# Kernel tuning notes

Hardware: AMD Instinct MI355X
Metric: run time of the kernel (lower is better)

Reference implementation:

```python
import jax, jax.numpy as jnp
import numpy as np

HIDDEN = 768
NUM_HEADS = 12
HEAD_DIM = HIDDEN // NUM_HEADS
B, S = 4, 2048


def setup_inputs() -> dict:
    key = jax.random.key(0)
    ks = jax.random.split(key, 10)
    scale = 1.0 / np.sqrt(HIDDEN)
    return {
        "hidden_states": jax.random.normal(ks[0], (B, S, HIDDEN), dtype=jnp.float32),
        "attention_mask": jnp.ones((B, S), dtype=jnp.float32),
        "Wq": jax.random.normal(ks[1], (HIDDEN, HIDDEN), dtype=jnp.float32) * scale,
        "bq": jnp.zeros((HIDDEN,), dtype=jnp.float32),
        "Wk": jax.random.normal(ks[2], (HIDDEN, HIDDEN), dtype=jnp.float32) * scale,
        "bk": jnp.zeros((HIDDEN,), dtype=jnp.float32),
        "Wv": jax.random.normal(ks[3], (HIDDEN, HIDDEN), dtype=jnp.float32) * scale,
        "bv": jnp.zeros((HIDDEN,), dtype=jnp.float32),
        "Wo": jax.random.normal(ks[4], (HIDDEN, HIDDEN), dtype=jnp.float32) * scale,
        "bo": jnp.zeros((HIDDEN,), dtype=jnp.float32),
    }


def reference(hidden_states, attention_mask, Wq, bq, Wk, bk, Wv, bv, Wo, bo):
    b, s, _ = hidden_states.shape
    # nn.Linear: x @ W.T + b  (W is [out, in])
    Q = hidden_states @ Wq.T + bq
    K = hidden_states @ Wk.T + bk
    V = hidden_states @ Wv.T + bv
    # [b, s, h*d] -> [b, h, s, d]
    Q = Q.reshape(b, s, NUM_HEADS, HEAD_DIM).transpose(0, 2, 1, 3)
    K = K.reshape(b, s, NUM_HEADS, HEAD_DIM).transpose(0, 2, 1, 3)
    V = V.reshape(b, s, NUM_HEADS, HEAD_DIM).transpose(0, 2, 1, 3)
    # scores: [b, h, s, s]
    scores = jnp.einsum("bhqd,bhkd->bhqk", Q, K) / jnp.sqrt(
        jnp.asarray(HEAD_DIM, dtype=Q.dtype))
    # mask: [b, s] -> additive bias broadcast over heads and query dim
    bias = (1.0 - attention_mask)[:, None, None, :] * -10000.0
    scores = scores + bias
    probs = jax.nn.softmax(scores, axis=-1)  # dropout p=0.0 -> identity
    context = jnp.einsum("bhqk,bhkd->bhqd", probs, V)
    context = context.transpose(0, 2, 1, 3).reshape(b, s, HIDDEN)
    return context @ Wo.T + bo
```

## Files before the change

### kernel.cpp

```cpp
#include <hip/hip_runtime.h>
#include <hip/hip_bf16.h>

#define SEQ   2048
#define NH    12
#define MTOK  8192

typedef __attribute__((ext_vector_type(8))) short short8;
typedef __attribute__((ext_vector_type(4))) short short4v;
typedef __attribute__((ext_vector_type(4))) float f32x4;

__device__ inline short f2bf(float x) {
  __hip_bfloat16 h = __float2bfloat16(x);
  return *(short*)&h;
}

#define GLL(gp, lp) __builtin_amdgcn_global_load_lds( \
    (const __attribute__((address_space(1))) void*)(gp), \
    (__attribute__((address_space(3))) void*)(lp), 16, 0, 0)

#define MFMA(a, b, c) __builtin_amdgcn_mfma_f32_16x16x32_bf16(a, b, c, 0, 0, 0)

#if !defined(__HIP_DEVICE_COMPILE__)
#define MFMA16(a, b, c) (c)
#elif __has_builtin(__builtin_amdgcn_mfma_f32_16x16x16bf16_1k)
#define MFMA16(a, b, c) __builtin_amdgcn_mfma_f32_16x16x16bf16_1k(a, b, c, 0, 0, 0)
#elif __has_builtin(__builtin_amdgcn_mfma_f32_16x16x16_bf16)
#define MFMA16(a, b, c) __builtin_amdgcn_mfma_f32_16x16x16_bf16(a, b, c, 0, 0, 0)
#else
#error "no 16x16x16 bf16 mfma builtin on device"
#endif

#if !defined(__HIP_DEVICE_COMPILE__)
#define EXP2(x) (x)
#elif __has_builtin(__builtin_amdgcn_exp2f)
#define EXP2(x) __builtin_amdgcn_exp2f(x)
#else
#define EXP2(x) __expf((x) * 0.6931471805599453f)
#endif

__device__ inline unsigned pack2bf(float a, float b) {
  unsigned ua = __float_as_uint(a) + 0x8000u;
  unsigned ub = __float_as_uint(b) + 0x8000u;
#if defined(__HIP_DEVICE_COMPILE__) && __has_builtin(__builtin_amdgcn_perm)
  return __builtin_amdgcn_perm(ub, ua, 0x07060302u);
#else
  return (ub & 0xFFFF0000u) | (ua >> 16);
#endif
}

__device__ inline unsigned packtrunc2(float a, float b) {
#if defined(__HIP_DEVICE_COMPILE__) && __has_builtin(__builtin_amdgcn_perm)
  return __builtin_amdgcn_perm(__float_as_uint(b), __float_as_uint(a),
                               0x07060302u);
#else
  return (__float_as_uint(b) & 0xFFFF0000u) | (__float_as_uint(a) >> 16);
#endif
}

union PackFrag {
  unsigned u[2];
  short4v s;
};

#define QSCALE 0.18033688011112042f
#define MBSCALE -14426.950408889634f

__global__ __launch_bounds__(256) void prep(
    const float* __restrict__ hs, const float* __restrict__ Wq,
    const float* __restrict__ Wk, const float* __restrict__ Wv,
    const float* __restrict__ Wo, const float* __restrict__ mask,
    short* __restrict__ Xb, short* __restrict__ Wqkvb,
    short* __restrict__ Wob, float* __restrict__ mbias) {
  int bid = blockIdx.x;
  if (bid < 6144) {
    int i = bid * 256 + threadIdx.x;
    float4 v = ((const float4*)hs)[i];
    short4v o;
    o[0] = f2bf(v.x); o[1] = f2bf(v.y); o[2] = f2bf(v.z); o[3] = f2bf(v.w);
    ((short4v*)Xb)[i] = o;
  } else if (bid < 6144 + 2304) {
    int idx = (bid - 6144) * 256 + threadIdx.x;
    int r = idx / 192, c = (idx - r * 192) * 4;
    const float* src;
    short* dst;
    int rr;
    if (r < 768)       { src = Wq; rr = r;        dst = Wqkvb; }
    else if (r < 1536) { src = Wk; rr = r - 768;  dst = Wqkvb; }
    else if (r < 2304) { src = Wv; rr = r - 1536; dst = Wqkvb; }
    else               { src = Wo; rr = r - 2304; dst = Wob; r = rr; }
    float4 v = *(const float4*)&src[(size_t)rr * 768 + c];
    short4v o;
    o[0] = f2bf(v.x); o[1] = f2bf(v.y); o[2] = f2bf(v.z); o[3] = f2bf(v.w);
    *(short4v*)&dst[(size_t)r * 768 + c] = o;
  } else {
    int i = (bid - 6144 - 2304) * 256 + threadIdx.x;
    if (i < MTOK) mbias[i] = (1.f - mask[i]) * MBSCALE;
  }
}

#define GEMM_BK64_LOOP(Aptr, Bptr)                                            \
  __shared__ __align__(16) short As[128 * 64];                                \
  __shared__ __align__(16) short Bs[128 * 64];                                \
  const int t = threadIdx.x;                                                  \
  const int wid = t >> 6, lane = t & 63, l15 = lane & 15, quad = lane >> 4;   \
  const int bm = blockIdx.x * 128, bn = blockIdx.y * 128;                     \
  const int mq = (wid & 1) * 64, nq = (wid >> 1) * 64;                        \
  const int srow8 = lane >> 3;                                                \
  const int schunk = lane & 7;                                                \
  const int scol = (schunk ^ srow8) * 8;                                      \
  f32x4 acc[4][4] = {};                                                       \
  const short *gA[4], *gB[4];                                                 \
  _Pragma("unroll") for (int g = 0; g < 4; ++g) {                             \
    int row = wid * 32 + g * 8 + srow8;                                       \
    gA[g] = (Aptr) + (size_t)(bm + row) * 768 + scol;                         \
    gB[g] = (Bptr) + (size_t)(bn + row) * 768 + scol;                         \
  }                                                                           \
  for (int k0 = 0; k0 < 768; k0 += 64) {                                      \
    _Pragma("unroll") for (int g = 0; g < 4; ++g)                             \
      GLL(gA[g] + k0, &As[(wid * 32 + g * 8) * 64]);                          \
    _Pragma("unroll") for (int g = 0; g < 4; ++g)                             \
      GLL(gB[g] + k0, &Bs[(wid * 32 + g * 8) * 64]);                          \
    __syncthreads();                                                          \
    _Pragma("unroll") for (int ks = 0; ks < 2; ++ks) {                        \
      short8 a[4], b[4];                                                      \
      _Pragma("unroll") for (int mt = 0; mt < 4; ++mt)                        \
        a[mt] = *(const short8*)&As[(mq + mt * 16 + l15) * 64 +               \
                                    (((ks * 4 + quad) ^ (l15 & 7)) * 8)];     \
      _Pragma("unroll") for (int nt = 0; nt < 4; ++nt)                        \
        b[nt] = *(const short8*)&Bs[(nq + nt * 16 + l15) * 64 +               \
                                    (((ks * 4 + quad) ^ (l15 & 7)) * 8)];     \
      _Pragma("unroll") for (int mt = 0; mt < 4; ++mt)                        \
        _Pragma("unroll") for (int nt = 0; nt < 4; ++nt)                      \
          acc[mt][nt] = MFMA(a[mt], b[nt], acc[mt][nt]);                      \
    }                                                                         \
    __syncthreads();                                                          \
  }

__global__ __launch_bounds__(256) void gemm_qkv(
    const short* __restrict__ A, const short* __restrict__ B,
    const float* __restrict__ bq, const float* __restrict__ bk,
    const float* __restrict__ bv, short* __restrict__ Qb,
    short* __restrict__ Kb, short* __restrict__ Vt) {
  GEMM_BK64_LOOP(A, B)

  const int seg = bn >= 1536 ? 2 : (bn >= 768 ? 1 : 0);
  const float* bias = seg == 0 ? bq : (seg == 1 ? bk : bv);
  const int colbase = bn - seg * 768;

  if (seg < 2) {
    short* dst = seg == 0 ? Qb : Kb;
    const float sc = seg == 0 ? QSCALE : 1.f;
#pragma unroll
    for (int mt = 0; mt < 4; ++mt)
#pragma unroll
      for (int nt = 0; nt < 4; ++nt) {
        int col = colbase + nq + nt * 16 + l15;
        float bias_v = bias[col];
#pragma unroll
        for (int i = 0; i < 4; ++i) {
          int row = bm + mq + mt * 16 + quad * 4 + i;
          dst[(size_t)row * 768 + col] = f2bf((acc[mt][nt][i] + bias_v) * sc);
        }
      }
  } else {
#pragma unroll
    for (int mt = 0; mt < 4; ++mt) {
      int row0 = bm + mq + mt * 16 + quad * 4;
      int b_ = row0 >> 11, s = row0 & 2047;
#pragma unroll
      for (int nt = 0; nt < 4; ++nt) {
        int col = colbase + nq + nt * 16 + l15;
        float bias_v = bias[col];
        int h = col >> 6, d = col & 63;
        short4v pv;
#pragma unroll
        for (int i = 0; i < 4; ++i) pv[i] = f2bf(acc[mt][nt][i] + bias_v);
        *(short4v*)&Vt[(((size_t)b_ * NH + h) * 64 + d) * 2048 + s] = pv;
      }
    }
  }
}

__global__ __launch_bounds__(256) void gemm_out(
    const short* __restrict__ A, const short* __restrict__ B,
    const float* __restrict__ bias, float* __restrict__ C) {
  GEMM_BK64_LOOP(A, B)

#pragma unroll
  for (int mt = 0; mt < 4; ++mt)
#pragma unroll
    for (int nt = 0; nt < 4; ++nt) {
      int col = bn + nq + nt * 16 + l15;
      float bias_v = bias[col];
#pragma unroll
      for (int i = 0; i < 4; ++i) {
        int row = bm + mq + mt * 16 + quad * 4 + i;
        C[(size_t)row * 768 + col] = acc[mt][nt][i] + bias_v;
      }
    }
}

__global__ __launch_bounds__(256, 3) void attn_v11(
    const short* __restrict__ Qb, const short* __restrict__ Kb,
    const short* __restrict__ Vt, const float* __restrict__ maskb,
    short* __restrict__ Ctx) {
  __shared__ __align__(16) short Ks[2][64 * 64];
  __shared__ __align__(16) short Vs[2][64 * 64];
  const int t = threadIdx.x;
  const int w = t >> 6, lane = t & 63, l15 = lane & 15, quad = lane >> 4;
  const int bh = blockIdx.x, b = bh / NH, h = bh % NH;
  const int q0 = blockIdx.y * 128;

  short8 qa[2][2];
#pragma unroll
  for (int qt = 0; qt < 2; ++qt)
#pragma unroll
    for (int ks = 0; ks < 2; ++ks) {
      int row = b * 2048 + q0 + w * 32 + qt * 16 + l15;
      qa[qt][ks] = *(const short8*)&Qb[(size_t)row * 768 + h * 64 + ks * 32 + quad * 8];
    }

  f32x4 O[2][4] = {};
  f32x4 lacc[2] = {};
  short4v ones4;
#pragma unroll
  for (int j = 0; j < 4; ++j) ones4[j] = (short)0x3F80;

  const int r0 = w * 16 + (lane >> 3);
  const int pc = lane & 7;
  const int swz0 = (pc ^ (r0 & 7)) * 8;
  const int swz1 = (pc ^ ((r0 + 8) & 7)) * 8;
  const short* gK0 = Kb + (size_t)(b * 2048 + r0) * 768 + h * 64 + swz0;
  const short* gK1 = Kb + (size_t)(b * 2048 + r0 + 8) * 768 + h * 64 + swz1;
  const short* gV0 = Vt + ((size_t)bh * 64 + r0) * 2048 + swz0;
  const short* gV1 = Vt + ((size_t)bh * 64 + r0 + 8) * 2048 + swz1;
  const float* mb = maskb + b * 2048;
  const int rs = l15 & 7;

  GLL(gK0, &Ks[0][(w * 16) * 64]);
  GLL(gK1, &Ks[0][(w * 16 + 8) * 64]);
  GLL(gV0, &Vs[0][(w * 16) * 64]);
  GLL(gV1, &Vs[0][(w * 16 + 8) * 64]);

  for (int ti = 0; ti < 32; ++ti) {
    const int cur = ti & 1;
    const int k0 = ti * 64;
    __syncthreads();

    {
      const size_t kn = (size_t)(((ti + 1) & 31) * 64);
      GLL(gK0 + kn * 768, &Ks[1 - cur][(w * 16) * 64]);
      GLL(gK1 + kn * 768, &Ks[1 - cur][(w * 16 + 8) * 64]);
      GLL(gV0 + kn, &Vs[1 - cur][(w * 16) * 64]);
      GLL(gV1 + kn, &Vs[1 - cur][(w * 16 + 8) * 64]);
    }

    f32x4 S[4][2];
#pragma unroll
    for (int kt = 0; kt < 4; ++kt) {
      float4 mb4 = *(const float4*)&mb[k0 + kt * 16 + quad * 4];
      f32x4 seed = {mb4.x, mb4.y, mb4.z, mb4.w};
      S[kt][0] = seed;
      S[kt][1] = seed;
    }
#pragma unroll
    for (int ks = 0; ks < 2; ++ks) {
      short8 kb[4];
#pragma unroll
      for (int kt = 0; kt < 4; ++kt)
        kb[kt] = *(const short8*)&Ks[cur][(kt * 16 + l15) * 64 +
                                         (((ks * 4 + quad) ^ rs) * 8)];
#pragma unroll
      for (int kt = 0; kt < 4; ++kt) {
        S[kt][0] = MFMA(kb[kt], qa[0][ks], S[kt][0]);
        S[kt][1] = MFMA(kb[kt], qa[1][ks], S[kt][1]);
      }
    }

    short4v pb[4][2];
#pragma unroll
    for (int kt = 0; kt < 4; ++kt) {
#pragma unroll
      for (int qt = 0; qt < 2; ++qt) {
        float p0 = EXP2(S[kt][qt][0]);
        float p1 = EXP2(S[kt][qt][1]);
        float p2 = EXP2(S[kt][qt][2]);
        float p3 = EXP2(S[kt][qt][3]);
        PackFrag pf;
        pf.u[0] = packtrunc2(p0, p1);
        pf.u[1] = packtrunc2(p2, p3);
        pb[kt][qt] = pf.s;
      }
    }

#pragma unroll
    for (int kt = 0; kt < 4; ++kt) {
      lacc[0] = MFMA16(ones4, pb[kt][0], lacc[0]);
      lacc[1] = MFMA16(ones4, pb[kt][1], lacc[1]);
    }

#pragma unroll
    for (int kt = 0; kt < 4; ++kt) {
#pragma unroll
      for (int dt = 0; dt < 4; ++dt) {
        short4v av = *(const short4v*)&Vs[cur][(dt * 16 + l15) * 64 +
            (((kt * 2 + (quad >> 1)) ^ rs) * 8) + (quad & 1) * 4];
        O[0][dt] = MFMA16(av, pb[kt][0], O[0][dt]);
        O[1][dt] = MFMA16(av, pb[kt][1], O[1][dt]);
      }
    }
  }

#pragma unroll
  for (int qt = 0; qt < 2; ++qt) {
    float inv = 1.f / lacc[qt][0];
    int row = b * 2048 + q0 + w * 32 + qt * 16 + l15;
#pragma unroll
    for (int dt = 0; dt < 4; ++dt) {
      PackFrag pf;
      pf.u[0] = pack2bf(O[qt][dt][0] * inv, O[qt][dt][1] * inv);
      pf.u[1] = pack2bf(O[qt][dt][2] * inv, O[qt][dt][3] * inv);
      *(short4v*)&Ctx[(size_t)row * 768 + h * 64 + dt * 16 + quad * 4] = pf.s;
    }
  }
}

extern "C" void kernel_launch(void* const* d_in, const int* in_sizes, int n_in,
                              void* d_out, int out_size, void* d_ws,
                              size_t ws_size, hipStream_t stream) {
  const float* hs   = (const float*)d_in[0];
  const float* mask = (const float*)d_in[1];
  const float* Wq   = (const float*)d_in[2];
  const float* bq   = (const float*)d_in[3];
  const float* Wk   = (const float*)d_in[4];
  const float* bk   = (const float*)d_in[5];
  const float* Wv   = (const float*)d_in[6];
  const float* bv   = (const float*)d_in[7];
  const float* Wo   = (const float*)d_in[8];
  const float* bo   = (const float*)d_in[9];

  char* ws = (char*)d_ws;
  short* Xb    = (short*)(ws);
  short* Wqkvb = (short*)(ws + 12582912);
  short* Wob   = (short*)(ws + 16121856);
  short* Qb    = (short*)(ws + 17301504);
  short* Kb    = (short*)(ws + 29884416);
  short* Vtg   = (short*)(ws + 42467328);
  short* Ctxb  = (short*)(ws + 55050240);
  float* mbias = (float*)(ws + 67633152);

  prep<<<8480, 256, 0, stream>>>(hs, Wq, Wk, Wv, Wo, mask,
                                 Xb, Wqkvb, Wob, mbias);
  gemm_qkv<<<dim3(64, 18), 256, 0, stream>>>(Xb, Wqkvb, bq, bk, bv,
                                             Qb, Kb, Vtg);
  attn_v11<<<dim3(48, 16), 256, 0, stream>>>(Qb, Kb, Vtg, mbias, Ctxb);
  gemm_out<<<dim3(64, 6), 256, 0, stream>>>(Ctxb, Wob, bo, (float*)d_out);
}
```

Measured before the change: 230.5 us.

## Switch attention to 32x32x16 MFMA tiles with permlane32 swap for P fragments

The attention kernel moves from 16x16x32/16x16x16 bf16 MFMAs to 32x32x16 bf16 MFMAs for QK^T, the row-sum accumulation and PV. Exponentiated scores are rearranged into B-operand fragments in registers with permlane32_swap rather than relying on the narrower 16x16x16 layout. The aim is fewer MFMA issues, fewer LDS reads per tile and denser matrix-core use. In exchange it needs larger accumulator register footprints and cross-lane swaps, which could affect occupancy.

```diff
diff --git a/kernel.cpp b/kernel.cpp
--- a/kernel.cpp
+++ b/kernel.cpp
@@ -8,6 +8,8 @@
 typedef __attribute__((ext_vector_type(8))) short short8;
 typedef __attribute__((ext_vector_type(4))) short short4v;
 typedef __attribute__((ext_vector_type(4))) float f32x4;
+typedef __attribute__((ext_vector_type(16))) float f32x16;
+typedef __attribute__((ext_vector_type(2))) unsigned uint2v;
 
 __device__ inline short f2bf(float x) {
   __hip_bfloat16 h = __float2bfloat16(x);
@@ -21,13 +23,9 @@
 #define MFMA(a, b, c) __builtin_amdgcn_mfma_f32_16x16x32_bf16(a, b, c, 0, 0, 0)
 
 #if !defined(__HIP_DEVICE_COMPILE__)
-#define MFMA16(a, b, c) (c)
-#elif __has_builtin(__builtin_amdgcn_mfma_f32_16x16x16bf16_1k)
-#define MFMA16(a, b, c) __builtin_amdgcn_mfma_f32_16x16x16bf16_1k(a, b, c, 0, 0, 0)
-#elif __has_builtin(__builtin_amdgcn_mfma_f32_16x16x16_bf16)
-#define MFMA16(a, b, c) __builtin_amdgcn_mfma_f32_16x16x16_bf16(a, b, c, 0, 0, 0)
-#else
-#error "no 16x16x16 bf16 mfma builtin on device"
+#define MFMA32(a, b, c) (c)
+#else
+#define MFMA32(a, b, c) __builtin_amdgcn_mfma_f32_32x32x16_bf16(a, b, c, 0, 0, 0)
 #endif
 
 #if !defined(__HIP_DEVICE_COMPILE__)
@@ -57,9 +55,29 @@
 #endif
 }
 
+__device__ inline uint2v lane32swap(unsigned a, unsigned b) {
+#if defined(__HIP_DEVICE_COMPILE__) && __has_builtin(__builtin_amdgcn_permlane32_swap)
+  return __builtin_amdgcn_permlane32_swap(a, b, false, false);
+#else
+  int lane = (int)(threadIdx.x & 63);
+  unsigned xa = (unsigned)__shfl((int)a, lane ^ 32, 64);
+  unsigned xb = (unsigned)__shfl((int)b, lane ^ 32, 64);
+  bool hi = lane >= 32;
+  uint2v r;
+  r.x = hi ? xb : a;
+  r.y = hi ? b : xa;
+  return r;
+#endif
+}
+
 union PackFrag {
   unsigned u[2];
   short4v s;
+};
+
+union Frag8 {
+  unsigned u[4];
+  short8 s;
 };
 
 #define QSCALE 0.18033688011112042f
@@ -200,31 +218,29 @@
     }
 }
 
-__global__ __launch_bounds__(256, 3) void attn_v11(
+__global__ __launch_bounds__(256, 3) void attn_v12(
     const short* __restrict__ Qb, const short* __restrict__ Kb,
     const short* __restrict__ Vt, const float* __restrict__ maskb,
     short* __restrict__ Ctx) {
   __shared__ __align__(16) short Ks[2][64 * 64];
   __shared__ __align__(16) short Vs[2][64 * 64];
   const int t = threadIdx.x;
-  const int w = t >> 6, lane = t & 63, l15 = lane & 15, quad = lane >> 4;
+  const int w = t >> 6, lane = t & 63, l31 = lane & 31, hi = lane >> 5;
   const int bh = blockIdx.x, b = bh / NH, h = bh % NH;
   const int q0 = blockIdx.y * 128;
 
-  short8 qa[2][2];
-#pragma unroll
-  for (int qt = 0; qt < 2; ++qt)
-#pragma unroll
-    for (int ks = 0; ks < 2; ++ks) {
-      int row = b * 2048 + q0 + w * 32 + qt * 16 + l15;
-      qa[qt][ks] = *(const short8*)&Qb[(size_t)row * 768 + h * 64 + ks * 32 + quad * 8];
-    }
-
-  f32x4 O[2][4] = {};
-  f32x4 lacc[2] = {};
-  short4v ones4;
-#pragma unroll
-  for (int j = 0; j < 4; ++j) ones4[j] = (short)0x3F80;
+  short8 qb[4];
+  {
+    int rowq = b * 2048 + q0 + w * 32 + l31;
+    const short* qp = &Qb[(size_t)rowq * 768 + h * 64 + hi * 8];
+#pragma unroll
+    for (int kc = 0; kc < 4; ++kc) qb[kc] = *(const short8*)&qp[kc * 16];
+  }
+
+  f32x16 O0 = {}, O1 = {}, lacc = {};
+  short8 ones8;
+#pragma unroll
+  for (int j = 0; j < 8; ++j) ones8[j] = (short)0x3F80;
 
   const int r0 = w * 16 + (lane >> 3);
   const int pc = lane & 7;
@@ -235,7 +251,7 @@
   const short* gV0 = Vt + ((size_t)bh * 64 + r0) * 2048 + swz0;
   const short* gV1 = Vt + ((size_t)bh * 64 + r0 + 8) * 2048 + swz1;
   const float* mb = maskb + b * 2048;
-  const int rs = l15 & 7;
+  const int rs = l31 & 7;
 
   GLL(gK0, &Ks[0][(w * 16) * 64]);
   GLL(gK1, &Ks[0][(w * 16 + 8) * 64]);
@@ -255,72 +271,73 @@
       GLL(gV1 + kn, &Vs[1 - cur][(w * 16 + 8) * 64]);
     }
 
-    f32x4 S[4][2];
-#pragma unroll
-    for (int kt = 0; kt < 4; ++kt) {
-      float4 mb4 = *(const float4*)&mb[k0 + kt * 16 + quad * 4];
-      f32x4 seed = {mb4.x, mb4.y, mb4.z, mb4.w};
-      S[kt][0] = seed;
-      S[kt][1] = seed;
-    }
-#pragma unroll
-    for (int ks = 0; ks < 2; ++ks) {
-      short8 kb[4];
-#pragma unroll
-      for (int kt = 0; kt < 4; ++kt)
-        kb[kt] = *(const short8*)&Ks[cur][(kt * 16 + l15) * 64 +
-                                         (((ks * 4 + quad) ^ rs) * 8)];
-#pragma unroll
-      for (int kt = 0; kt < 4; ++kt) {
-        S[kt][0] = MFMA(kb[kt], qa[0][ks], S[kt][0]);
-        S[kt][1] = MFMA(kb[kt], qa[1][ks], S[kt][1]);
-      }
-    }
-
-    short4v pb[4][2];
-#pragma unroll
-    for (int kt = 0; kt < 4; ++kt) {
-#pragma unroll
-      for (int qt = 0; qt < 2; ++qt) {
-        float p0 = EXP2(S[kt][qt][0]);
-        float p1 = EXP2(S[kt][qt][1]);
-        float p2 = EXP2(S[kt][qt][2]);
-        float p3 = EXP2(S[kt][qt][3]);
-        PackFrag pf;
-        pf.u[0] = packtrunc2(p0, p1);
-        pf.u[1] = packtrunc2(p2, p3);
-        pb[kt][qt] = pf.s;
-      }
-    }
-
-#pragma unroll
-    for (int kt = 0; kt < 4; ++kt) {
-      lacc[0] = MFMA16(ones4, pb[kt][0], lacc[0]);
-      lacc[1] = MFMA16(ones4, pb[kt][1], lacc[1]);
-    }
-
-#pragma unroll
-    for (int kt = 0; kt < 4; ++kt) {
-#pragma unroll
-      for (int dt = 0; dt < 4; ++dt) {
-        short4v av = *(const short4v*)&Vs[cur][(dt * 16 + l15) * 64 +
-            (((kt * 2 + (quad >> 1)) ^ rs) * 8) + (quad & 1) * 4];
-        O[0][dt] = MFMA16(av, pb[kt][0], O[0][dt]);
-        O[1][dt] = MFMA16(av, pb[kt][1], O[1][dt]);
-      }
-    }
-  }
-
-#pragma unroll
-  for (int qt = 0; qt < 2; ++qt) {
-    float inv = 1.f / lacc[qt][0];
-    int row = b * 2048 + q0 + w * 32 + qt * 16 + l15;
-#pragma unroll
-    for (int dt = 0; dt < 4; ++dt) {
-      PackFrag pf;
-      pf.u[0] = pack2bf(O[qt][dt][0] * inv, O[qt][dt][1] * inv);
-      pf.u[1] = pack2bf(O[qt][dt][2] * inv, O[qt][dt][3] * inv);
-      *(short4v*)&Ctx[(size_t)row * 768 + h * 64 + dt * 16 + quad * 4] = pf.s;
+    short8 pfrag[4];
+
+#pragma unroll
+    for (int kb2 = 0; kb2 < 2; ++kb2) {
+      f32x16 S;
+#pragma unroll
+      for (int g = 0; g < 4; ++g) {
+        float4 m4 = *(const float4*)&mb[k0 + kb2 * 32 + g * 8 + hi * 4];
+        S[4 * g + 0] = m4.x; S[4 * g + 1] = m4.y;
+        S[4 * g + 2] = m4.z; S[4 * g + 3] = m4.w;
+      }
+#pragma unroll
+      for (int kc = 0; kc < 4; ++kc) {
+        short8 ka = *(const short8*)&Ks[cur][(kb2 * 32 + l31) * 64 +
+                                            (((kc * 2 + hi) ^ rs) * 8)];
+        S = MFMA32(ka, qb[kc], S);
+      }
+      unsigned pk[4][2];
+#pragma unroll
+      for (int g = 0; g < 4; ++g) {
+        float p0 = EXP2(S[4 * g + 0]);
+        float p1 = EXP2(S[4 * g + 1]);
+        float p2 = EXP2(S[4 * g + 2]);
+        float p3 = EXP2(S[4 * g + 3]);
+        pk[g][0] = packtrunc2(p0, p1);
+        pk[g][1] = packtrunc2(p2, p3);
+      }
+#pragma unroll
+      for (int half = 0; half < 2; ++half) {
+        Frag8 f;
+        uint2v ra = lane32swap(pk[half * 2][0], pk[half * 2 + 1][0]);
+        uint2v rb = lane32swap(pk[half * 2][1], pk[half * 2 + 1][1]);
+        f.u[0] = ra.x;
+        f.u[1] = rb.x;
+        f.u[2] = ra.y;
+        f.u[3] = rb.y;
+        pfrag[kb2 * 2 + half] = f.s;
+      }
+    }
+
+#pragma unroll
+    for (int c = 0; c < 4; ++c) lacc = MFMA32(ones8, pfrag[c], lacc);
+
+#pragma unroll
+    for (int c = 0; c < 4; ++c) {
+      short8 av0 = *(const short8*)&Vs[cur][(l31) * 64 +
+                                           (((c * 2 + hi) ^ rs) * 8)];
+      short8 av1 = *(const short8*)&Vs[cur][(32 + l31) * 64 +
+                                           (((c * 2 + hi) ^ rs) * 8)];
+      O0 = MFMA32(av0, pfrag[c], O0);
+      O1 = MFMA32(av1, pfrag[c], O1);
+    }
+  }
+
+  {
+    float inv = 1.f / lacc[0];
+    int rowq = b * 2048 + q0 + w * 32 + l31;
+    short* cp = &Ctx[(size_t)rowq * 768 + h * 64 + hi * 4];
+#pragma unroll
+    for (int g = 0; g < 4; ++g) {
+      PackFrag pf0, pf1;
+      pf0.u[0] = pack2bf(O0[4 * g + 0] * inv, O0[4 * g + 1] * inv);
+      pf0.u[1] = pack2bf(O0[4 * g + 2] * inv, O0[4 * g + 3] * inv);
+      *(short4v*)&cp[g * 8] = pf0.s;
+      pf1.u[0] = pack2bf(O1[4 * g + 0] * inv, O1[4 * g + 1] * inv);
+      pf1.u[1] = pack2bf(O1[4 * g + 2] * inv, O1[4 * g + 3] * inv);
+      *(short4v*)&cp[32 + g * 8] = pf1.s;
     }
   }
 }
@@ -353,6 +370,6 @@
                                  Xb, Wqkvb, Wob, mbias);
   gemm_qkv<<<dim3(64, 18), 256, 0, stream>>>(Xb, Wqkvb, bq, bk, bv,
                                              Qb, Kb, Vtg);
-  attn_v11<<<dim3(48, 16), 256, 0, stream>>>(Qb, Kb, Vtg, mbias, Ctxb);
+  attn_v12<<<dim3(48, 16), 256, 0, stream>>>(Qb, Kb, Vtg, mbias, Ctxb);
   gemm_out<<<dim3(64, 6), 256, 0, stream>>>(Ctxb, Wob, bo, (float*)d_out);
 }
```

After: 231.5 us. About the same (+0.4%).
